# Kernel tuning notes

Hardware: AMD Instinct MI355X
Metric: run time of the kernel (lower is better)

## Reference

```python
import jax, jax.numpy as jnp
import numpy as np
from jax import lax

# dims: B=16, T=1500, E(enc)=512, D(dec)=512, A(att_dim)=512, C(out_channels)=10, K(kernel)=201, H(heads)=4
SHARPENING = 1.0


def setup_inputs() -> dict:
    key = jax.random.key(0)
    ks = jax.random.split(key, 12)
    B, T, E, D, A, C, K, H = 16, 1500, 512, 512, 512, 10, 201, 4
    s = 0.02
    return {
        "enc_out": jax.random.normal(ks[0], (B, T, E), dtype=jnp.float32),
        "x_lens": jax.random.randint(ks[1], (B,), 1, T + 1, dtype=jnp.int32),
        "dec_out": jax.random.normal(ks[2], (B, 1, D), dtype=jnp.float32),
        "aw_step": jax.random.uniform(ks[3], (B, T, H), dtype=jnp.float32),
        "W_enc": jax.random.normal(ks[4], (H, E, A), dtype=jnp.float32) * s,
        "b_enc": jnp.zeros((H, A), dtype=jnp.float32),
        "W_dec": jax.random.normal(ks[5], (H, D, A), dtype=jnp.float32) * s,
        "W_conv": jax.random.normal(ks[6], (H, C, A), dtype=jnp.float32) * s,
        "conv_w": jax.random.normal(ks[7], (H, C, K), dtype=jnp.float32) * s,
        "v": jax.random.normal(ks[8], (H, A), dtype=jnp.float32) * s,
        "W_mha": jax.random.normal(ks[9], (H * E, E), dtype=jnp.float32) * s,
        "b_mha": jnp.zeros((E,), dtype=jnp.float32),
    }


def reference(enc_out, x_lens, dec_out, aw_step, W_enc, b_enc, W_dec, W_conv, conv_w, v, W_mha, b_mha):
    B, T, E = enc_out.shape
    H, C, K = conv_w.shape
    # per-head encoder projection (cached enc_out_a in original): [B,T,H,A]
    enc_a = jnp.einsum('bte,hea->btha', enc_out, W_enc) + b_enc
    # per-head decoder projection, broadcast over T: [B,1,H,A]
    dec_a = jnp.einsum('bqd,hda->bqha', dec_out, W_dec)
    # location features: per-head 1D conv over T of previous attention weights
    lhs = jnp.transpose(aw_step, (0, 2, 1))          # [B,H,T]
    rhs = conv_w.reshape(H * C, 1, K)                # grouped conv, one group per head
    conv = lax.conv_general_dilated(lhs, rhs, (1,), 'SAME',
                                    dimension_numbers=('NCH', 'OIH', 'NCH'),
                                    feature_group_count=H)  # [B,H*C,T]
    conv = conv.reshape(B, H, C, T)
    conv_a = jnp.einsum('bhct,hca->btha', conv, W_conv)      # [B,T,H,A]
    # additive energy: v^T tanh(enc + dec + conv) per head -> [B,T,H]
    energy = jnp.einsum('btha,ha->bth', jnp.tanh(enc_a + dec_a + conv_a), v)
    # original multiplies energy by 0/1 mask (NOT -inf) before softmax over T
    mask = (jnp.arange(T)[None, :] < x_lens[:, None]).astype(energy.dtype)  # [B,T]
    energy = energy * mask[:, :, None] * SHARPENING
    aw = jax.nn.softmax(energy, axis=1)                      # softmax over T per head
    # per-head context, heads concatenated along feature dim: [B,1,H*E]
    ctx = jnp.einsum('bte,bth->bhe', enc_out, aw).reshape(B, 1, H * E)
    context_vec = ctx @ W_mha + b_mha                        # [B,1,E]
    return context_vec, aw
```

## Files before the change

kernel.cpp:

```cpp
#include <hip/hip_runtime.h>
#include <hip/hip_bf16.h>

#define B_ 16
#define T_ 1500
#define E_ 512
#define A_ 512
#define H_ 4
#define C_ 10
#define K_ 201
#define M_ (B_*T_)
#define KW_ 544

typedef __attribute__((ext_vector_type(8))) short short8v;
typedef __attribute__((ext_vector_type(4))) float f32x4;
typedef __attribute__((ext_vector_type(4))) unsigned short ushort4v;
typedef __attribute__((ext_vector_type(8))) unsigned short ushort8v;

typedef __attribute__((address_space(1))) const char gch;
typedef __attribute__((address_space(3))) char lch;

__device__ __forceinline__ void gload16(const void* g, void* l) {
    __builtin_amdgcn_global_load_lds((gch*)g, (lch*)l, 16, 0, 0);
}

__device__ inline unsigned short f2bf(float x) {
    unsigned int u = __float_as_uint(x);
    return (unsigned short)((u + 0x7fffu + ((u >> 16) & 1u)) >> 16);
}

__global__ void k_prep(const float* __restrict__ enc, unsigned short* __restrict__ encB,
                       const float* __restrict__ Wenc, const float* __restrict__ Wconv,
                       unsigned short* __restrict__ WencTp,
                       const float* __restrict__ dec, const float* __restrict__ Wdec,
                       const float* __restrict__ benc, float* __restrict__ decA,
                       float* __restrict__ out,
                       const float* __restrict__ aw_step, const float* __restrict__ conv_w,
                       unsigned short* __restrict__ convA, float* __restrict__ wszero) {
    __shared__ float smemf[4456];
    int bid = blockIdx.x;
    int tid = threadIdx.x;

    if (bid < 6000) {
        int i = bid * 256 + tid;
        const float4* src = (const float4*)enc + (size_t)i * 2;
        float4 f0 = src[0], f1 = src[1];
        ushort8v o = { f2bf(f0.x), f2bf(f0.y), f2bf(f0.z), f2bf(f0.w),
                       f2bf(f1.x), f2bf(f1.y), f2bf(f1.z), f2bf(f1.w) };
        *(ushort8v*)&encB[(size_t)i * 8] = o;
        return;
    }
    if (bid < 7088) {
        int idx = bid - 6000;
        int bx = idx & 15, by = (idx >> 4) % 17, h = idx / 272;
        int tx = tid & 31, ty = tid >> 5;
        if (by == 16) {
            int base = (h * 16 + bx) * 1024;
            #pragma unroll
            for (int k = 0; k < 4; k++) {
                int i2 = base + k * 256 + tid;
                int c = i2 & 31, n = (i2 >> 5) & 511, hh = i2 >> 14;
                float val = (c < C_) ? Wconv[(hh * C_ + c) * A_ + n] : 0.0f;
                WencTp[((size_t)(hh * A_ + n)) * KW_ + 512 + c] = f2bf(val);
            }
            return;
        }
        float (*tile)[33] = (float(*)[33])smemf;
        int e0 = bx * 32, a0 = by * 32;
        const float* src = Wenc + h * E_ * A_;
        #pragma unroll
        for (int i = 0; i < 4; i++) tile[ty + i*8][tx] = src[(e0 + ty + i*8) * A_ + a0 + tx];
        __syncthreads();
        unsigned short* dst = WencTp + (size_t)h * A_ * KW_;
        #pragma unroll
        for (int i = 0; i < 4; i++) dst[(size_t)(a0 + ty + i*8) * KW_ + e0 + tx] = f2bf(tile[tx][ty + i*8]);
        return;
    }
    if (bid < 7152) {
        int bh = bid - 7088, b = bh >> 2, h = bh & 3;
        int a = tid;
        if (bh < 32) out[bh * 256 + a] = 0.0f;
        float acc0 = 0.f, acc1 = 0.f;
        const float* W = Wdec + h * E_ * A_;
        const float* x = dec + b * 512;
        for (int d = 0; d < 512; d++) {
            float s = x[d];
            acc0 += s * W[d * A_ + a];
            acc1 += s * W[d * A_ + a + 256];
        }
        decA[bh * A_ + a]       = acc0 + benc[h * A_ + a];
        decA[bh * A_ + a + 256] = acc1 + benc[h * A_ + a + 256];
        return;
    }
    {
        int i = bid - 7152;
        int b = i & 15, h = (i >> 4) & 3, tc = i >> 6;
        int t0 = tc * 250;
        float* seg = smemf;
        unsigned short* outl = (unsigned short*)(smemf + 456);
        {
            int idx = (i * 256 + tid) * 2;
            if (idx < 128768)     wszero[idx] = 0.0f;
            if (idx + 1 < 128768) wszero[idx + 1] = 0.0f;
        }
        for (int idx = tid; idx < 450; idx += 256) {
            int tt = t0 - 100 + idx;
            seg[idx] = (tt >= 0 && tt < T_) ? aw_step[(b * T_ + tt) * H_ + h] : 0.0f;
        }
        for (int idx = tid; idx < 8000; idx += 256) outl[idx] = 0;
        __syncthreads();
        if (tid < 250) {
            float acc[10] = {0,0,0,0,0,0,0,0,0,0};
            const float* cw = conv_w + h * C_ * K_;
            for (int k = 0; k < K_; k++) {
                float sv = seg[tid + k];
                #pragma unroll
                for (int c = 0; c < 10; c++) acc[c] += sv * cw[c * K_ + k];
            }
            #pragma unroll
            for (int c = 0; c < 10; c++) outl[tid * 32 + c] = f2bf(acc[c]);
        }
        __syncthreads();
        unsigned short* dst = convA + ((size_t)h * M_ + (size_t)b * T_ + t0) * 32;
        for (int idx = tid; idx < 2000; idx += 256)
            *(ushort4v*)&dst[idx * 4] = *(const ushort4v*)&outl[idx * 4];
    }
}

__launch_bounds__(256, 3)
__global__ void k_energy(const unsigned short* __restrict__ encB,
                         const unsigned short* __restrict__ WencTp,
                         const unsigned short* __restrict__ convA,
                         const float* __restrict__ decA,
                         const float* __restrict__ v,
                         float* __restrict__ energy) {
    __shared__ unsigned short As[3][4096];
    __shared__ unsigned short Bs[3][4096];
    int m0 = blockIdx.x * 128;
    int h  = blockIdx.y >> 2;
    int n0 = (blockIdx.y & 3) * 128;
    int tid = threadIdx.x;
    int lane = tid & 63, w = tid >> 6;
    int wr = w >> 1, wc = w & 1;
    int lc = lane & 15, lr16 = lane >> 4;

    int srow  = lane >> 2;
    int sslot = (lane & 3) ^ ((lane >> 3) & 3);

    const char* pa[2]; const char* pb[2]; const char* pca[2];
    #pragma unroll
    for (int i = 0; i < 2; i++) {
        int c = i * 4 + w;
        int row = c * 16 + srow;
        int grow = min(m0 + row, M_ - 1);
        pa[i]  = (const char*)encB + ((size_t)grow * 512 + sslot * 8) * 2;
        pb[i]  = (const char*)WencTp + ((size_t)(h * 512 + n0 + row) * KW_ + sslot * 8) * 2;
        pca[i] = (const char*)convA + (((size_t)h * M_ + grow) * 32 + sslot * 8) * 2;
    }

    int kslot = (lr16 ^ ((lc >> 1) & 3)) * 8;

    f32x4 acc[4][4] = {};

    #pragma unroll
    for (int i = 0; i < 2; i++) {
        int c = i * 4 + w;
        gload16(pa[i],      (char*)As[0] + c * 1024);
        gload16(pb[i],      (char*)Bs[0] + c * 1024);
        gload16(pa[i] + 64, (char*)As[1] + c * 1024);
        gload16(pb[i] + 64, (char*)Bs[1] + c * 1024);
    }

    int bc = 0, bn1 = 1, bn2 = 2;
    for (int s = 0; s < 17; ++s) {
        int t = s + 2;
        if (t <= 16) {
            #pragma unroll
            for (int i = 0; i < 2; i++) {
                int c = i * 4 + w;
                const char* asrc = (t < 16) ? pa[i] + t * 64 : pca[i];
                gload16(asrc,            (char*)As[bn2] + c * 1024);
                gload16(pb[i] + t * 64,  (char*)Bs[bn2] + c * 1024);
            }
        }
        if (s <= 14)      asm volatile("s_waitcnt vmcnt(8)" ::: "memory");
        else if (s == 15) asm volatile("s_waitcnt vmcnt(4)" ::: "memory");
        else              asm volatile("s_waitcnt vmcnt(0)" ::: "memory");
        __builtin_amdgcn_s_barrier();
        __builtin_amdgcn_sched_barrier(0);
        {
            short8v a[4], b[4];
            #pragma unroll
            for (int mi = 0; mi < 4; mi++)
                a[mi] = *(const short8v*)&As[bc][(wr * 64 + mi * 16 + lc) * 32 + kslot];
            #pragma unroll
            for (int ni = 0; ni < 4; ni++)
                b[ni] = *(const short8v*)&Bs[bc][(wc * 64 + ni * 16 + lc) * 32 + kslot];
            #pragma unroll
            for (int mi = 0; mi < 4; mi++)
                #pragma unroll
                for (int ni = 0; ni < 4; ni++)
                    acc[mi][ni] = __builtin_amdgcn_mfma_f32_16x16x32_bf16(b[ni], a[mi], acc[mi][ni], 0, 0, 0);
        }
        __builtin_amdgcn_sched_barrier(0);
        __builtin_amdgcn_s_barrier();
        int tmp = bc; bc = bn1; bn1 = bn2; bn2 = tmp;
    }

    #pragma unroll
    for (int mi = 0; mi < 4; mi++) {
        int mrow = m0 + wr * 64 + mi * 16 + lc;
        if (mrow < M_) {
            int bb = mrow / 1500;
            const float* dA = decA + (bb * 4 + h) * 512;
            float s = 0.f;
            #pragma unroll
            for (int ni = 0; ni < 4; ni++) {
                #pragma unroll
                for (int r = 0; r < 4; r++) {
                    int n = n0 + wc * 64 + ni * 16 + lr16 * 4 + r;
                    float xv = acc[mi][ni][r] + dA[n];
                    float tt = __builtin_amdgcn_rcpf(__expf(2.0f * xv) + 1.0f);
                    float vv = v[h * 512 + n];
                    s += __builtin_fmaf(-2.0f * tt, vv, vv);
                }
            }
            s += __shfl_xor(s, 16);
            s += __shfl_xor(s, 32);
            if (lr16 == 0) atomicAdd(&energy[(size_t)mrow * 4 + h], s);
        }
    }
}

__global__ void k_softmax(const float* __restrict__ energy, const int* __restrict__ xlens,
                          float* __restrict__ aw) {
    __shared__ float red[8];
    int b = blockIdx.x, h = blockIdx.y;
    int tid = threadIdx.x;
    int len = xlens[b];
    float e[6];
    float m = -1e30f;
    #pragma unroll
    for (int i = 0; i < 6; i++) {
        int t = tid + i * 256;
        float val = 0.0f;
        if (t < T_) {
            val = (t < len) ? energy[(size_t)(b * T_ + t) * H_ + h] : 0.0f;
            m = fmaxf(m, val);
        }
        e[i] = val;
    }
    #pragma unroll
    for (int mk = 1; mk < 64; mk <<= 1) m = fmaxf(m, __shfl_xor(m, mk));
    if ((tid & 63) == 0) red[tid >> 6] = m;
    __syncthreads();
    m = fmaxf(fmaxf(red[0], red[1]), fmaxf(red[2], red[3]));
    float ssum = 0.f;
    #pragma unroll
    for (int i = 0; i < 6; i++) {
        int t = tid + i * 256;
        if (t < T_) { e[i] = expf(e[i] - m); ssum += e[i]; }
    }
    #pragma unroll
    for (int mk = 1; mk < 64; mk <<= 1) ssum += __shfl_xor(ssum, mk);
    if ((tid & 63) == 0) red[4 + (tid >> 6)] = ssum;
    __syncthreads();
    float inv = 1.0f / (red[4] + red[5] + red[6] + red[7]);
    #pragma unroll
    for (int i = 0; i < 6; i++) {
        int t = tid + i * 256;
        if (t < T_) aw[(size_t)(b * T_ + t) * H_ + h] = e[i] * inv;
    }
}

__global__ void k_ctx(const unsigned short* __restrict__ encB, const float* __restrict__ aw,
                      float* __restrict__ ctx) {
    __shared__ float s_aw[500];
    int b = blockIdx.x, tc = blockIdx.y;
    int t0 = tc * 125;
    int tid = threadIdx.x;
    for (int idx = tid; idx < 500; idx += 256)
        s_aw[idx] = aw[(size_t)b * T_ * H_ + t0 * H_ + idx];
    __syncthreads();
    int e = tid * 2;
    float a00=0,a01=0,a10=0,a11=0,a20=0,a21=0,a30=0,a31=0;
    for (int tl = 0; tl < 125; tl++) {
        unsigned int u = *(const unsigned int*)&encB[(size_t)(b * T_ + t0 + tl) * E_ + e];
        float e0 = __uint_as_float((u & 0xffffu) << 16);
        float e1 = __uint_as_float(u & 0xffff0000u);
        float w0 = s_aw[tl*4+0], w1 = s_aw[tl*4+1], w2 = s_aw[tl*4+2], w3 = s_aw[tl*4+3];
        a00 += e0*w0; a01 += e1*w0; a10 += e0*w1; a11 += e1*w1;
        a20 += e0*w2; a21 += e1*w2; a30 += e0*w3; a31 += e1*w3;
    }
    atomicAdd(&ctx[b*2048 + 0*512 + e],   a00); atomicAdd(&ctx[b*2048 + 0*512 + e+1], a01);
    atomicAdd(&ctx[b*2048 + 1*512 + e],   a10); atomicAdd(&ctx[b*2048 + 1*512 + e+1], a11);
    atomicAdd(&ctx[b*2048 + 2*512 + e],   a20); atomicAdd(&ctx[b*2048 + 2*512 + e+1], a21);
    atomicAdd(&ctx[b*2048 + 3*512 + e],   a30); atomicAdd(&ctx[b*2048 + 3*512 + e+1], a31);
}

__global__ void k_proj(const float* __restrict__ ctx, const float* __restrict__ Wmha,
                       const float* __restrict__ bmha, float* __restrict__ out) {
    __shared__ float s_c[256];
    int b = blockIdx.x, ic = blockIdx.y;
    int tid = threadIdx.x;
    if (tid < 256) s_c[tid] = ctx[b * 2048 + ic * 256 + tid];
    __syncthreads();
    float acc = (ic == 0) ? bmha[tid] : 0.0f;
    const float* W = Wmha + (size_t)ic * 256 * 512;
    for (int i = 0; i < 256; i++) acc += s_c[i] * W[i * 512 + tid];
    atomicAdd(&out[b * 512 + tid], acc);
}

extern "C" void kernel_launch(void* const* d_in, const int* in_sizes, int n_in,
                              void* d_out, int out_size, void* d_ws, size_t ws_size,
                              hipStream_t stream) {
    const float* enc   = (const float*)d_in[0];
    const int*   xlens = (const int*)  d_in[1];
    const float* dec   = (const float*)d_in[2];
    const float* aw_st = (const float*)d_in[3];
    const float* Wenc  = (const float*)d_in[4];
    const float* benc  = (const float*)d_in[5];
    const float* Wdec  = (const float*)d_in[6];
    const float* Wconv = (const float*)d_in[7];
    const float* convw = (const float*)d_in[8];
    const float* v     = (const float*)d_in[9];
    const float* Wmha  = (const float*)d_in[10];
    const float* bmha  = (const float*)d_in[11];
    float* out = (float*)d_out;

    char* ws = (char*)d_ws;
    float* energy          = (float*)(ws);
    float* ctx             = (float*)(ws + 384000);
    float* decA            = (float*)(ws + 515072);
    unsigned short* WencTp = (unsigned short*)(ws + 646144);
    unsigned short* convA  = (unsigned short*)(ws + 2874368);
    unsigned short* encB   = (unsigned short*)(ws + 9018368);
    float* aw = out + 8192;

    k_prep    <<<7536, 256, 0, stream>>>(enc, encB, Wenc, Wconv, WencTp,
                                         dec, Wdec, benc, decA, out,
                                         aw_st, convw, convA, (float*)ws);
    k_energy  <<<dim3(188, 16), 256, 0, stream>>>(encB, WencTp, convA, decA, v, energy);
    k_softmax <<<dim3(16, 4), 256, 0, stream>>>(energy, xlens, aw);
    k_ctx     <<<dim3(16, 12), 256, 0, stream>>>(encB, aw, ctx);
    k_proj    <<<dim3(16, 8), 512, 0, stream>>>(ctx, Wmha, bmha, out);
}
```

Baseline: 152.2 us.

## Fuse softmax into context kernel and use one barrier per GEMM k-step

Drops the separate softmax launch. Each context block now loads its batch's full energy row into shared memory, recomputes the per-head max and sum itself, and writes the attention weights for its own time chunk. Separately, the energy GEMM main loop waits and synchronises once at the top of each iteration instead of twice, rotating its triple buffer with modular counters, so it carries one fewer barrier per k-step. The cost is that all twelve blocks per batch recompute the same softmax reductions, and shared memory per context block grows to about 26 KB.

```diff
diff --git a/kernel.cpp b/kernel.cpp
--- a/kernel.cpp
+++ b/kernel.cpp
@@ -170,23 +170,23 @@
         gload16(pb[i] + 64, (char*)Bs[1] + c * 1024);
     }
 
-    int bc = 0, bn1 = 1, bn2 = 2;
+    int bc = 0, bn2 = 2;
     for (int s = 0; s < 17; ++s) {
+        if (s < 16) asm volatile("s_waitcnt vmcnt(4)" ::: "memory");
+        else        asm volatile("s_waitcnt vmcnt(0)" ::: "memory");
+        __builtin_amdgcn_s_barrier();
+        __builtin_amdgcn_sched_barrier(0);
         int t = s + 2;
         if (t <= 16) {
             #pragma unroll
             for (int i = 0; i < 2; i++) {
                 int c = i * 4 + w;
                 const char* asrc = (t < 16) ? pa[i] + t * 64 : pca[i];
-                gload16(asrc,            (char*)As[bn2] + c * 1024);
-                gload16(pb[i] + t * 64,  (char*)Bs[bn2] + c * 1024);
+                const char* bsrc = (t < 16) ? pb[i] + t * 64 : pb[i] + 16 * 64;
+                gload16(asrc, (char*)As[bn2] + c * 1024);
+                gload16(bsrc, (char*)Bs[bn2] + c * 1024);
             }
         }
-        if (s <= 14)      asm volatile("s_waitcnt vmcnt(8)" ::: "memory");
-        else if (s == 15) asm volatile("s_waitcnt vmcnt(4)" ::: "memory");
-        else              asm volatile("s_waitcnt vmcnt(0)" ::: "memory");
-        __builtin_amdgcn_s_barrier();
-        __builtin_amdgcn_sched_barrier(0);
         {
             short8v a[4], b[4];
             #pragma unroll
@@ -202,8 +202,8 @@
                     acc[mi][ni] = __builtin_amdgcn_mfma_f32_16x16x32_bf16(b[ni], a[mi], acc[mi][ni], 0, 0, 0);
         }
         __builtin_amdgcn_sched_barrier(0);
-        __builtin_amdgcn_s_barrier();
-        int tmp = bc; bc = bn1; bn1 = bn2; bn2 = tmp;
+        bc  = (bc  == 2) ? 0 : bc + 1;
+        bn2 = (bn2 == 2) ? 0 : bn2 + 1;
     }
 
     #pragma unroll
@@ -231,55 +231,42 @@
     }
 }
 
-__global__ void k_softmax(const float* __restrict__ energy, const int* __restrict__ xlens,
-                          float* __restrict__ aw) {
-    __shared__ float red[8];
-    int b = blockIdx.x, h = blockIdx.y;
-    int tid = threadIdx.x;
-    int len = xlens[b];
-    float e[6];
-    float m = -1e30f;
-    #pragma unroll
-    for (int i = 0; i < 6; i++) {
-        int t = tid + i * 256;
-        float val = 0.0f;
-        if (t < T_) {
-            val = (t < len) ? energy[(size_t)(b * T_ + t) * H_ + h] : 0.0f;
-            m = fmaxf(m, val);
-        }
-        e[i] = val;
-    }
-    #pragma unroll
-    for (int mk = 1; mk < 64; mk <<= 1) m = fmaxf(m, __shfl_xor(m, mk));
-    if ((tid & 63) == 0) red[tid >> 6] = m;
-    __syncthreads();
-    m = fmaxf(fmaxf(red[0], red[1]), fmaxf(red[2], red[3]));
-    float ssum = 0.f;
-    #pragma unroll
-    for (int i = 0; i < 6; i++) {
-        int t = tid + i * 256;
-        if (t < T_) { e[i] = expf(e[i] - m); ssum += e[i]; }
-    }
-    #pragma unroll
-    for (int mk = 1; mk < 64; mk <<= 1) ssum += __shfl_xor(ssum, mk);
-    if ((tid & 63) == 0) red[4 + (tid >> 6)] = ssum;
-    __syncthreads();
-    float inv = 1.0f / (red[4] + red[5] + red[6] + red[7]);
-    #pragma unroll
-    for (int i = 0; i < 6; i++) {
-        int t = tid + i * 256;
-        if (t < T_) aw[(size_t)(b * T_ + t) * H_ + h] = e[i] * inv;
-    }
-}
-
-__global__ void k_ctx(const unsigned short* __restrict__ encB, const float* __restrict__ aw,
-                      float* __restrict__ ctx) {
+__global__ void k_ctx(const unsigned short* __restrict__ encB,
+                      const float* __restrict__ energy,
+                      const int* __restrict__ xlens,
+                      float* __restrict__ aw, float* __restrict__ ctx) {
+    __shared__ float sE[6000];
     __shared__ float s_aw[500];
+    __shared__ float sMS[8];
     int b = blockIdx.x, tc = blockIdx.y;
     int t0 = tc * 125;
     int tid = threadIdx.x;
-    for (int idx = tid; idx < 500; idx += 256)
-        s_aw[idx] = aw[(size_t)b * T_ * H_ + t0 * H_ + idx];
+    int len = xlens[b];
+    const float* eb = energy + (size_t)b * 6000;
+    for (int idx = tid; idx < 6000; idx += 256) {
+        int t = idx >> 2;
+        sE[idx] = (t < len) ? eb[idx] : 0.0f;
+    }
+    __syncthreads();
+    {
+        int wv = tid >> 6, lane = tid & 63;
+        float m = -1e30f;
+        for (int i = lane; i < T_; i += 64) m = fmaxf(m, sE[i * 4 + wv]);
+        #pragma unroll
+        for (int mk = 1; mk < 64; mk <<= 1) m = fmaxf(m, __shfl_xor(m, mk));
+        float ssum = 0.f;
+        for (int i = lane; i < T_; i += 64) ssum += __expf(sE[i * 4 + wv] - m);
+        #pragma unroll
+        for (int mk = 1; mk < 64; mk <<= 1) ssum += __shfl_xor(ssum, mk);
+        if (lane == 0) { sMS[wv] = m; sMS[4 + wv] = 1.0f / ssum; }
+    }
+    __syncthreads();
+    for (int idx = tid; idx < 500; idx += 256) {
+        int hh = idx & 3;
+        float av = __expf(sE[t0 * 4 + idx] - sMS[hh]) * sMS[4 + hh];
+        s_aw[idx] = av;
+        aw[(size_t)b * 6000 + t0 * 4 + idx] = av;
+    }
     __syncthreads();
     int e = tid * 2;
     float a00=0,a01=0,a10=0,a11=0,a20=0,a21=0,a30=0,a31=0;
@@ -336,11 +323,10 @@
     unsigned short* encB   = (unsigned short*)(ws + 9018368);
     float* aw = out + 8192;
 
-    k_prep    <<<7536, 256, 0, stream>>>(enc, encB, Wenc, Wconv, WencTp,
-                                         dec, Wdec, benc, decA, out,
-                                         aw_st, convw, convA, (float*)ws);
-    k_energy  <<<dim3(188, 16), 256, 0, stream>>>(encB, WencTp, convA, decA, v, energy);
-    k_softmax <<<dim3(16, 4), 256, 0, stream>>>(energy, xlens, aw);
-    k_ctx     <<<dim3(16, 12), 256, 0, stream>>>(encB, aw, ctx);
-    k_proj    <<<dim3(16, 8), 512, 0, stream>>>(ctx, Wmha, bmha, out);
-}
+    k_prep   <<<7536, 256, 0, stream>>>(enc, encB, Wenc, Wconv, WencTp,
+                                        dec, Wdec, benc, decA, out,
+                                        aw_st, convw, convA, (float*)ws);
+    k_energy <<<dim3(188, 16), 256, 0, stream>>>(encB, WencTp, convA, decA, v, energy);
+    k_ctx    <<<dim3(16, 12), 256, 0, stream>>>(encB, energy, xlens, aw, ctx);
+    k_proj   <<<dim3(16, 8), 512, 0, stream>>>(ctx, Wmha, bmha, out);
+}
```

Result: no change. 155.0 us (+1.9%).

## Compute two heads per energy GEMM block to reuse encoder A tiles

Applied to the files above, without the earlier changes.

Each k_energy block now computes two heads at once, sharing the loaded encoder tile across two weight tiles. This halves the grid and halves encoder re-reads from global memory. The location-conv features for a head pair are packed into a 64-wide K tail, so KW grows to 576 and the K loop gets one extra step. The pipeline is also reordered to wait and barrier before issuing the next prefetch, dropping the trailing barrier. In exchange, register use doubles, the launch bound drops to 2 waves per SIMD, and LDS use rises, which may reduce occupancy.

```diff
diff --git a/kernel.cpp b/kernel.cpp
--- a/kernel.cpp
+++ b/kernel.cpp
@@ -9,7 +9,7 @@
 #define C_ 10
 #define K_ 201
 #define M_ (B_*T_)
-#define KW_ 544
+#define KW_ 576
 
 typedef __attribute__((ext_vector_type(8))) short short8v;
 typedef __attribute__((ext_vector_type(4))) float f32x4;
@@ -35,7 +35,7 @@
                        const float* __restrict__ benc, float* __restrict__ decA,
                        float* __restrict__ out,
                        const float* __restrict__ aw_step, const float* __restrict__ conv_w,
-                       unsigned short* __restrict__ convA, float* __restrict__ wszero) {
+                       unsigned short* __restrict__ convAB, float* __restrict__ wszero) {
     __shared__ float smemf[4456];
     int bid = blockIdx.x;
     int tid = threadIdx.x;
@@ -54,13 +54,15 @@
         int bx = idx & 15, by = (idx >> 4) % 17, h = idx / 272;
         int tx = tid & 31, ty = tid >> 5;
         if (by == 16) {
-            int base = (h * 16 + bx) * 1024;
-            #pragma unroll
-            for (int k = 0; k < 4; k++) {
+            int base = (h * 16 + bx) * 2048;
+            #pragma unroll
+            for (int k = 0; k < 8; k++) {
                 int i2 = base + k * 256 + tid;
-                int c = i2 & 31, n = (i2 >> 5) & 511, hh = i2 >> 14;
-                float val = (c < C_) ? Wconv[(hh * C_ + c) * A_ + n] : 0.0f;
-                WencTp[((size_t)(hh * A_ + n)) * KW_ + 512 + c] = f2bf(val);
+                int c6 = i2 & 63, n = (i2 >> 6) & 511, hh = i2 >> 15;
+                int own = ((c6 >> 5) == (hh & 1));
+                int ch = c6 & 31;
+                float val = (own && ch < C_) ? Wconv[(hh * C_ + ch) * A_ + n] : 0.0f;
+                WencTp[((size_t)(hh * A_ + n)) * KW_ + 512 + c6] = f2bf(val);
             }
             return;
         }
@@ -120,24 +122,28 @@
             for (int c = 0; c < 10; c++) outl[tid * 32 + c] = f2bf(acc[c]);
         }
         __syncthreads();
-        unsigned short* dst = convA + ((size_t)h * M_ + (size_t)b * T_ + t0) * 32;
-        for (int idx = tid; idx < 2000; idx += 256)
-            *(ushort4v*)&dst[idx * 4] = *(const ushort4v*)&outl[idx * 4];
-    }
-}
-
-__launch_bounds__(256, 3)
+        unsigned short* dst = convAB + ((size_t)(h >> 1) * M_ + (size_t)b * T_ + t0) * 64 + (h & 1) * 32;
+        for (int idx = tid; idx < 2000; idx += 256) {
+            int row = idx >> 3, q = idx & 7;
+            *(ushort4v*)&dst[row * 64 + q * 4] = *(const ushort4v*)&outl[row * 32 + q * 4];
+        }
+    }
+}
+
+__launch_bounds__(256, 2)
 __global__ void k_energy(const unsigned short* __restrict__ encB,
                          const unsigned short* __restrict__ WencTp,
-                         const unsigned short* __restrict__ convA,
+                         const unsigned short* __restrict__ convAB,
                          const float* __restrict__ decA,
                          const float* __restrict__ v,
                          float* __restrict__ energy) {
-    __shared__ unsigned short As[3][4096];
-    __shared__ unsigned short Bs[3][4096];
+    __shared__ unsigned short As [3][4096];
+    __shared__ unsigned short BsA[3][4096];
+    __shared__ unsigned short BsB[3][4096];
     int m0 = blockIdx.x * 128;
-    int h  = blockIdx.y >> 2;
+    int hp = blockIdx.y >> 2;
     int n0 = (blockIdx.y & 3) * 128;
+    int h0 = hp * 2, h1 = h0 + 1;
     int tid = threadIdx.x;
     int lane = tid & 63, w = tid >> 6;
     int wr = w >> 1, wc = w & 1;
@@ -146,87 +152,99 @@
     int srow  = lane >> 2;
     int sslot = (lane & 3) ^ ((lane >> 3) & 3);
 
-    const char* pa[2]; const char* pb[2]; const char* pca[2];
+    const char* pa[2]; const char* pbA[2]; const char* pbB[2]; const char* pca[2];
     #pragma unroll
     for (int i = 0; i < 2; i++) {
         int c = i * 4 + w;
         int row = c * 16 + srow;
         int grow = min(m0 + row, M_ - 1);
         pa[i]  = (const char*)encB + ((size_t)grow * 512 + sslot * 8) * 2;
-        pb[i]  = (const char*)WencTp + ((size_t)(h * 512 + n0 + row) * KW_ + sslot * 8) * 2;
-        pca[i] = (const char*)convA + (((size_t)h * M_ + grow) * 32 + sslot * 8) * 2;
+        pbA[i] = (const char*)WencTp + ((size_t)(h0 * 512 + n0 + row) * KW_ + sslot * 8) * 2;
+        pbB[i] = (const char*)WencTp + ((size_t)(h1 * 512 + n0 + row) * KW_ + sslot * 8) * 2;
+        pca[i] = (const char*)convAB + (((size_t)hp * M_ + grow) * 64 + sslot * 8) * 2;
     }
 
     int kslot = (lr16 ^ ((lc >> 1) & 3)) * 8;
 
-    f32x4 acc[4][4] = {};
+    f32x4 accA[4][4] = {};
+    f32x4 accB[4][4] = {};
 
     #pragma unroll
     for (int i = 0; i < 2; i++) {
         int c = i * 4 + w;
-        gload16(pa[i],      (char*)As[0] + c * 1024);
-        gload16(pb[i],      (char*)Bs[0] + c * 1024);
-        gload16(pa[i] + 64, (char*)As[1] + c * 1024);
-        gload16(pb[i] + 64, (char*)Bs[1] + c * 1024);
-    }
-
-    int bc = 0, bn1 = 1, bn2 = 2;
-    for (int s = 0; s < 17; ++s) {
+        gload16(pa[i],       (char*)As[0]  + c * 1024);
+        gload16(pbA[i],      (char*)BsA[0] + c * 1024);
+        gload16(pbB[i],      (char*)BsB[0] + c * 1024);
+        gload16(pa[i] + 64,  (char*)As[1]  + c * 1024);
+        gload16(pbA[i] + 64, (char*)BsA[1] + c * 1024);
+        gload16(pbB[i] + 64, (char*)BsB[1] + c * 1024);
+    }
+
+    int bc = 0, bn2 = 2;
+    for (int s = 0; s < 18; ++s) {
+        if (s < 17) asm volatile("s_waitcnt vmcnt(6)" ::: "memory");
+        else        asm volatile("s_waitcnt vmcnt(0)" ::: "memory");
+        __builtin_amdgcn_s_barrier();
+        __builtin_amdgcn_sched_barrier(0);
         int t = s + 2;
-        if (t <= 16) {
+        if (t <= 17) {
             #pragma unroll
             for (int i = 0; i < 2; i++) {
                 int c = i * 4 + w;
-                const char* asrc = (t < 16) ? pa[i] + t * 64 : pca[i];
-                gload16(asrc,            (char*)As[bn2] + c * 1024);
-                gload16(pb[i] + t * 64,  (char*)Bs[bn2] + c * 1024);
-            }
-        }
-        if (s <= 14)      asm volatile("s_waitcnt vmcnt(8)" ::: "memory");
-        else if (s == 15) asm volatile("s_waitcnt vmcnt(4)" ::: "memory");
-        else              asm volatile("s_waitcnt vmcnt(0)" ::: "memory");
-        __builtin_amdgcn_s_barrier();
-        __builtin_amdgcn_sched_barrier(0);
+                const char* asrc = (t < 16) ? pa[i] + t * 64 : pca[i] + (t - 16) * 64;
+                gload16(asrc,           (char*)As[bn2]  + c * 1024);
+                gload16(pbA[i] + t * 64, (char*)BsA[bn2] + c * 1024);
+                gload16(pbB[i] + t * 64, (char*)BsB[bn2] + c * 1024);
+            }
+        }
         {
-            short8v a[4], b[4];
+            short8v a[4], bA[4], bB[4];
             #pragma unroll
             for (int mi = 0; mi < 4; mi++)
                 a[mi] = *(const short8v*)&As[bc][(wr * 64 + mi * 16 + lc) * 32 + kslot];
             #pragma unroll
-            for (int ni = 0; ni < 4; ni++)
-                b[ni] = *(const short8v*)&Bs[bc][(wc * 64 + ni * 16 + lc) * 32 + kslot];
+            for (int ni = 0; ni < 4; ni++) {
+                bA[ni] = *(const short8v*)&BsA[bc][(wc * 64 + ni * 16 + lc) * 32 + kslot];
+                bB[ni] = *(const short8v*)&BsB[bc][(wc * 64 + ni * 16 + lc) * 32 + kslot];
+            }
             #pragma unroll
             for (int mi = 0; mi < 4; mi++)
                 #pragma unroll
-                for (int ni = 0; ni < 4; ni++)
-                    acc[mi][ni] = __builtin_amdgcn_mfma_f32_16x16x32_bf16(b[ni], a[mi], acc[mi][ni], 0, 0, 0);
+                for (int ni = 0; ni < 4; ni++) {
+                    accA[mi][ni] = __builtin_amdgcn_mfma_f32_16x16x32_bf16(bA[ni], a[mi], accA[mi][ni], 0, 0, 0);
+                    accB[mi][ni] = __builtin_amdgcn_mfma_f32_16x16x32_bf16(bB[ni], a[mi], accB[mi][ni], 0, 0, 0);
+                }
         }
         __builtin_amdgcn_sched_barrier(0);
-        __builtin_amdgcn_s_barrier();
-        int tmp = bc; bc = bn1; bn1 = bn2; bn2 = tmp;
-    }
-
-    #pragma unroll
-    for (int mi = 0; mi < 4; mi++) {
-        int mrow = m0 + wr * 64 + mi * 16 + lc;
-        if (mrow < M_) {
-            int bb = mrow / 1500;
-            const float* dA = decA + (bb * 4 + h) * 512;
-            float s = 0.f;
-            #pragma unroll
-            for (int ni = 0; ni < 4; ni++) {
+        bc  = (bc  == 2) ? 0 : bc + 1;
+        bn2 = (bn2 == 2) ? 0 : bn2 + 1;
+    }
+
+    #pragma unroll
+    for (int hd = 0; hd < 2; hd++) {
+        int h = h0 + hd;
+        #pragma unroll
+        for (int mi = 0; mi < 4; mi++) {
+            int mrow = m0 + wr * 64 + mi * 16 + lc;
+            if (mrow < M_) {
+                int bb = mrow / 1500;
+                const float* dA = decA + (bb * 4 + h) * 512;
+                float s = 0.f;
                 #pragma unroll
-                for (int r = 0; r < 4; r++) {
-                    int n = n0 + wc * 64 + ni * 16 + lr16 * 4 + r;
-                    float xv = acc[mi][ni][r] + dA[n];
-                    float tt = __builtin_amdgcn_rcpf(__expf(2.0f * xv) + 1.0f);
-                    float vv = v[h * 512 + n];
-                    s += __builtin_fmaf(-2.0f * tt, vv, vv);
+                for (int ni = 0; ni < 4; ni++) {
+                    #pragma unroll
+                    for (int r = 0; r < 4; r++) {
+                        int n = n0 + wc * 64 + ni * 16 + lr16 * 4 + r;
+                        float xv = (hd ? accB[mi][ni][r] : accA[mi][ni][r]) + dA[n];
+                        float tt = __builtin_amdgcn_rcpf(__expf(2.0f * xv) + 1.0f);
+                        float vv = v[h * 512 + n];
+                        s += __builtin_fmaf(-2.0f * tt, vv, vv);
+                    }
                 }
-            }
-            s += __shfl_xor(s, 16);
-            s += __shfl_xor(s, 32);
-            if (lr16 == 0) atomicAdd(&energy[(size_t)mrow * 4 + h], s);
+                s += __shfl_xor(s, 16);
+                s += __shfl_xor(s, 32);
+                if (lr16 == 0) atomicAdd(&energy[(size_t)mrow * 4 + h], s);
+            }
         }
     }
 }
@@ -332,14 +350,14 @@
     float* ctx             = (float*)(ws + 384000);
     float* decA            = (float*)(ws + 515072);
     unsigned short* WencTp = (unsigned short*)(ws + 646144);
-    unsigned short* convA  = (unsigned short*)(ws + 2874368);
-    unsigned short* encB   = (unsigned short*)(ws + 9018368);
+    unsigned short* convAB = (unsigned short*)(ws + 3005440);
+    unsigned short* encB   = (unsigned short*)(ws + 9149440);
     float* aw = out + 8192;
 
     k_prep    <<<7536, 256, 0, stream>>>(enc, encB, Wenc, Wconv, WencTp,
                                          dec, Wdec, benc, decA, out,
-                                         aw_st, convw, convA, (float*)ws);
-    k_energy  <<<dim3(188, 16), 256, 0, stream>>>(encB, WencTp, convA, decA, v, energy);
+                                         aw_st, convw, convAB, (float*)ws);
+    k_energy  <<<dim3(188, 8), 256, 0, stream>>>(encB, WencTp, convAB, decA, v, energy);
     k_softmax <<<dim3(16, 4), 256, 0, stream>>>(energy, xlens, aw);
     k_ctx     <<<dim3(16, 12), 256, 0, stream>>>(encB, aw, ctx);
     k_proj    <<<dim3(16, 8), 512, 0, stream>>>(ctx, Wmha, bmha, out);
```

Result: no change. 153.0 us (+0.6%).
